# Performance work log

Hardware: AMD Instinct MI355X
Metric: run time of the kernel (lower is better)

## Reference

```python
import jax, jax.numpy as jnp
import numpy as np

B, S, H, I, E, TOPK, KS = 4, 4096, 1024, 512, 16, 2, 3


def setup_inputs() -> dict:
    key = jax.random.key(0)
    ks = jax.random.split(key, 9)
    sc = 0.02
    return {
        "hidden_states": jax.random.normal(ks[0], (B, S, H), dtype=jnp.float32),
        "router_w": jax.random.normal(ks[1], (H, E), dtype=jnp.float32) * sc,
        "router_bias": jnp.zeros((E,), dtype=jnp.float32),
        "expert_gate_w": jax.random.normal(ks[2], (E - 1, H, I), dtype=jnp.float32) * sc,
        "expert_up_w": jax.random.normal(ks[3], (E - 1, H, I), dtype=jnp.float32) * sc,
        "expert_down_w": jax.random.normal(ks[4], (E - 1, I, H), dtype=jnp.float32) * sc,
        "conv_w": jax.random.normal(ks[5], (I, H, KS), dtype=jnp.float32) * sc,
        "shared_up_w": jax.random.normal(ks[6], (H, I), dtype=jnp.float32) * sc,
        "shared_down_w": jax.random.normal(ks[7], (I, H), dtype=jnp.float32) * sc,
    }


def reference(hidden_states, router_w, router_bias, expert_gate_w, expert_up_w,
              expert_down_w, conv_w, shared_up_w, shared_down_w):
    b, s, h = hidden_states.shape
    flat = hidden_states.reshape(b * s, h)  # (T, H)

    # ---- Router (mlp type, temperature=1, no noise at eval) ----
    logits = (flat @ router_w).astype(jnp.float32) + router_bias  # (T, E)
    probs = jax.nn.softmax(logits, axis=-1)
    top_w, top_i = jax.lax.top_k(probs, TOPK)  # (T, K)
    norm_w = top_w / (jnp.sum(top_w, axis=-1, keepdims=True) + 1e-6)
    norm_w = norm_w.astype(hidden_states.dtype)
    # Dense combine weights (T, E): scatter top-k weights into expert slots
    combine = jnp.sum(jax.nn.one_hot(top_i, E, dtype=norm_w.dtype) * norm_w[..., None], axis=1)

    # ---- Routed experts: E-1 SwiGLU MLPs + 1 Identity (index E-1) ----
    routed = combine[:, E - 1:E] * flat  # identity expert contribution
    for e in range(E - 1):
        y = (jax.nn.silu(flat @ expert_gate_w[e]) * (flat @ expert_up_w[e])) @ expert_down_w[e]
        routed = routed + combine[:, e:e + 1] * y
    routed = routed.reshape(b, s, h)

    # ---- Shared expert: causal conv1d gate * up, then down ----
    x_ncw = jnp.transpose(hidden_states, (0, 2, 1))  # (B, H, S)
    gate = jax.lax.conv_general_dilated(
        x_ncw, conv_w, window_strides=(1,), padding=[(KS - 1, 0)],
        dimension_numbers=("NCW", "OIW", "NCW"))  # (B, I, S)
    gate = jnp.transpose(gate, (0, 2, 1))  # (B, S, I)
    shared = (jax.nn.silu(gate) * (hidden_states @ shared_up_w)) @ shared_down_w

    return shared + routed
```

## Files before the change

### kernel.cpp

```cpp
#include <hip/hip_runtime.h>

typedef unsigned short u16;
typedef __attribute__((ext_vector_type(4))) float f32x4;
using bf16x8 = __attribute__((ext_vector_type(8))) short;
typedef __attribute__((ext_vector_type(8))) unsigned short u16x8;
typedef __attribute__((ext_vector_type(4))) unsigned short u16x4;

#define GAS __attribute__((address_space(1)))
#define LAS __attribute__((address_space(3)))

__device__ __forceinline__ float bf2f(u16 u) {
  unsigned v = ((unsigned)u) << 16;
  float f;
  __builtin_memcpy(&f, &v, 4);
  return f;
}
__device__ __forceinline__ u16 f2bf(float f) {
  unsigned u;
  __builtin_memcpy(&u, &f, 4);
  u += 0x7fffu + ((u >> 16) & 1u);
  return (u16)(u >> 16);
}
__device__ __forceinline__ void llds16(const void* g, void* l) {
  __builtin_amdgcn_global_load_lds((const GAS unsigned*)g, (LAS unsigned*)l, 16, 0, 0);
}

__global__ __launch_bounds__(256) void router_k(const float* __restrict__ x,
    const float* __restrict__ rw, const float* __restrict__ rb,
    int* __restrict__ topk_idx, float* __restrict__ topk_w, int* __restrict__ ib,
    u16* __restrict__ xb) {
  __shared__ float xs[4][32 * 65];
  __shared__ float wsm[4][32 * 16];
  __shared__ float part[4][64 * 17];
  __shared__ int cnt[16];
  const int tid = threadIdx.x;
  const int wv = __builtin_amdgcn_readfirstlane(tid >> 6);
  const int lane = tid & 63;
  const int tok0 = blockIdx.x * 64;
  const int rr = lane >> 3;
  const int c4 = (lane & 7) * 4;

  float acc[16];
#pragma unroll
  for (int e = 0; e < 16; ++e) acc[e] = 0.f;

  for (int c = 0; c < 8; ++c) {
    const int hb = wv * 256 + c * 32;
    {
      f32x4 wa = *(const f32x4*)(rw + hb * 16 + lane * 4);
      f32x4 wb = *(const f32x4*)(rw + hb * 16 + 256 + lane * 4);
      *(f32x4*)&wsm[wv][lane * 4] = wa;
      *(f32x4*)&wsm[wv][256 + lane * 4] = wb;
    }
#pragma unroll
    for (int i = 0; i < 8; ++i) {
      const int row = i * 8 + rr;
      const long gb = (long)(tok0 + row) * 1024 + hb + c4;
      f32x4 v = *(const f32x4*)(x + gb);
      u16x4 b4;
#pragma unroll
      for (int j = 0; j < 4; ++j) {
        xs[wv][(c4 + j) * 65 + row] = v[j];
        b4[j] = f2bf(v[j]);
      }
      *(u16x4*)(xb + gb) = b4;
    }
    __syncthreads();
#pragma unroll
    for (int h = 0; h < 32; ++h) {
      const float xv = xs[wv][h * 65 + lane];
      const float* wrow = &wsm[wv][h * 16];
#pragma unroll
      for (int q = 0; q < 4; ++q) {
        f32x4 w4 = *(const f32x4*)(wrow + q * 4);
#pragma unroll
        for (int e = 0; e < 4; ++e) acc[q * 4 + e] += xv * w4[e];
      }
    }
    __syncthreads();
  }
#pragma unroll
  for (int e = 0; e < 16; ++e) part[wv][lane * 17 + e] = acc[e];
  if (tid < 16) cnt[tid] = 0;
  __syncthreads();
  if (tid < 64) {
    float p[16];
#pragma unroll
    for (int e = 0; e < 16; ++e)
      p[e] = part[0][tid * 17 + e] + part[1][tid * 17 + e] +
             part[2][tid * 17 + e] + part[3][tid * 17 + e] + rb[e];
    float mx = p[0];
#pragma unroll
    for (int e = 1; e < 16; ++e) mx = fmaxf(mx, p[e]);
    float sum = 0.f;
#pragma unroll
    for (int e = 0; e < 16; ++e) { p[e] = __expf(p[e] - mx); sum += p[e]; }
    int i0 = 0; float p0 = p[0];
    for (int e = 1; e < 16; ++e) if (p[e] > p0) { p0 = p[e]; i0 = e; }
    int i1 = -1; float p1 = -1.f;
    for (int e = 0; e < 16; ++e) if (e != i0 && p[e] > p1) { p1 = p[e]; i1 = e; }
    const float inv = 1.f / sum;
    p0 *= inv; p1 *= inv;
    const float d = p0 + p1 + 1e-6f;
    const int t = tok0 + tid;
    topk_idx[t * 2] = i0; topk_idx[t * 2 + 1] = i1;
    topk_w[t * 2] = p0 / d;
    topk_w[t * 2 + 1] = p1 / d;
    if (i0 < 15) atomicAdd(&cnt[i0], 1);
    if (i1 < 15) atomicAdd(&cnt[i1], 1);
  }
  __syncthreads();
  if (tid < 15 && cnt[tid] > 0) atomicAdd(&ib[tid], cnt[tid]);
}

__global__ void zero_k(int* __restrict__ ib) {
  if (threadIdx.x < 16) ib[threadIdx.x] = 0;
}

__global__ void scan_k(int* __restrict__ ib) {
  if (threadIdx.x != 0 || blockIdx.x != 0) return;
  int off = 0;
  for (int ee = 0; ee < 15; ++ee) { ib[16 + ee] = off; ib[32 + ee] = off; off += ib[ee]; }
  ib[16 + 15] = off;
  int nm = 0;
  for (int ee = 0; ee < 15; ++ee) {
    const int st = ib[16 + ee], en = ib[16 + ee + 1];
    for (int r = st; r < en; r += 128) {
      ib[64 + nm * 4] = ee; ib[64 + nm * 4 + 1] = r; ib[64 + nm * 4 + 2] = en; ++nm;
    }
  }
  ib[48] = nm;
}

__global__ __launch_bounds__(256) void scatter_k(const int* __restrict__ topk_idx,
                          const float* __restrict__ topk_w,
                          int* __restrict__ ib, int* __restrict__ tok_ids,
                          float* __restrict__ tok_w, int* __restrict__ slot_map) {
  __shared__ int cnt[16], base[16];
  const int tid = threadIdx.x;
  const int j = blockIdx.x * 256 + tid;
  if (tid < 16) cnt[tid] = 0;
  __syncthreads();
  const int e = topk_idx[j];
  int lo = 0;
  if (e < 15) lo = atomicAdd(&cnt[e], 1);
  __syncthreads();
  if (tid < 15 && cnt[tid] > 0) base[tid] = atomicAdd(&ib[32 + tid], cnt[tid]);
  __syncthreads();
  if (e < 15) {
    const int pos = base[e] + lo;
    tok_ids[pos] = j >> 1;
    tok_w[pos] = topk_w[j];
    slot_map[j] = pos;
  } else {
    slot_map[j] = -1;
  }
}

__global__ void transpose_k(const float* __restrict__ src, u16* __restrict__ dst, int R, int C) {
  __shared__ float tile[32][33];
  src += (long)blockIdx.z * R * C;
  dst += (long)blockIdx.z * R * C;
  const int c0 = blockIdx.x * 32, r0 = blockIdx.y * 32;
  const int tx = threadIdx.x & 31, ty = threadIdx.x >> 5;
#pragma unroll
  for (int i = ty; i < 32; i += 8) tile[i][tx] = src[(long)(r0 + i) * C + c0 + tx];
  __syncthreads();
#pragma unroll
  for (int i = ty; i < 32; i += 8) dst[(long)(c0 + i) * R + r0 + tx] = f2bf(tile[tx][i]);
}

__global__ void convt_k(const float* __restrict__ cw, u16* __restrict__ dst) {
  const int idx = blockIdx.x * 256 + threadIdx.x;
  if (idx >= 3 * 512 * 1024) return;
  const int k = idx >> 19;
  const int rem = idx & 524287;
  const int i = rem >> 10, h = rem & 1023;
  dst[idx] = f2bf(cw[i * 3072 + h * 3 + k]);
}

template<int V>
__global__ __launch_bounds__(256, 2)
void gemm_k(const u16* __restrict__ Abase, const u16* __restrict__ Bt0,
            const u16* __restrict__ Bt1, void* __restrict__ OUTv,
            const int* __restrict__ tbl, const int* __restrict__ nmt,
            const int* __restrict__ tok_ids, const float* __restrict__ tok_w,
            int K, int ldA, int ldOut) {
  __shared__ u16 lds[24576];
  u16* OUT = (u16*)OUTv;
  float* OUTF = (float*)OUTv;
  const int tid = threadIdx.x;
  const int wave = tid >> 6, lane = tid & 63;
  const int quad = lane >> 4, l16 = lane & 15;
  const int rA = tid >> 2;
  const int sub8 = (tid & 3) * 8;
  const int sub8s = ((tid & 3) ^ ((tid >> 3) & 3)) * 8;

  constexpr int NYC = (V == 3) ? 4 : 8;
  const int lin = (blockIdx.x & 7) * (gridDim.x >> 3) + (blockIdx.x >> 3);
  const int bx = lin / NYC, by = lin - bx * NYC;

  int e = 0, row0, row_end;
  if constexpr (V <= 1) {
    if (bx >= *nmt) return;
    e = tbl[bx * 4]; row0 = tbl[bx * 4 + 1]; row_end = tbl[bx * 4 + 2];
  } else {
    row0 = bx * 128; row_end = row0 + 128;
  }
  const int n0 = by * ((V == 0) ? 64 : 128);

  f32x4 acc[2][8];
  f32x4 acc2[2][8];
#pragma unroll
  for (int i = 0; i < 2; ++i)
#pragma unroll
    for (int j = 0; j < 8; ++j) {
      acc[i][j] = (f32x4){0.f, 0.f, 0.f, 0.f};
      if constexpr (V == 3) acc2[i][j] = (f32x4){0.f, 0.f, 0.f, 0.f};
    }

  const int swz8 = (((l16 >> 1) & 3) ^ quad) * 8;
  const int aoff0 = (wave * 32 + l16) * 32 + swz8;
  const int aoff1 = aoff0 + 512;
  const int kIters = K / 32;

  if constexpr (V != 3) {
    const u16 *pA0, *pA1, *pB0, *pB1;
    if constexpr (V == 0) {
      const int t0i = tok_ids[min(row0 + rA, row_end - 1)];
      const int t1i = tok_ids[min(row0 + rA + 64, row_end - 1)];
      pA0 = Abase + (long)t0i * 1024 + sub8s;
      pA1 = Abase + (long)t1i * 1024 + sub8s;
      pB0 = Bt0 + ((long)e * 512 + n0 + rA) * 1024 + sub8s;
      pB1 = Bt1 + ((long)e * 512 + n0 + rA) * 1024 + sub8s;
    } else if constexpr (V == 1) {
      pA0 = Abase + (long)min(row0 + rA, row_end - 1) * 512 + sub8s;
      pA1 = Abase + (long)min(row0 + rA + 64, row_end - 1) * 512 + sub8s;
      pB0 = Bt0 + ((long)e * 1024 + n0 + rA) * 512 + sub8s;
      pB1 = Bt0 + ((long)e * 1024 + n0 + rA + 64) * 512 + sub8s;
    } else {
      pA0 = Abase + (long)(row0 + rA) * ldA + sub8s;
      pA1 = Abase + (long)(row0 + rA + 64) * ldA + sub8s;
      pB0 = Bt0 + (long)(n0 + rA) * K + sub8s;
      pB1 = Bt0 + (long)(n0 + rA + 64) * K + sub8s;
    }
    auto STAGE = [&](int buf) {
      llds16(pA0, &lds[buf + wave * 512]); pA0 += 32;
      llds16(pA1, &lds[buf + 2048 + wave * 512]); pA1 += 32;
      llds16(pB0, &lds[buf + 4096 + wave * 512]); pB0 += 32;
      llds16(pB1, &lds[buf + 6144 + wave * 512]); pB1 += 32;
    };
    STAGE(0);
    STAGE(8192);
    int cur = 0, stg = 16384;
    for (int kb = 0; kb < kIters; ++kb) {
      if (kb + 1 < kIters) {
        asm volatile("s_waitcnt vmcnt(4)" ::: "memory");
      } else {
        asm volatile("s_waitcnt vmcnt(0)" ::: "memory");
      }
      __builtin_amdgcn_s_barrier();
      if (kb + 2 < kIters) {
        STAGE(stg);
        stg = (stg == 16384) ? 0 : stg + 8192;
      }
      bf16x8 a0 = *(const bf16x8*)&lds[cur + aoff0];
      bf16x8 a1 = *(const bf16x8*)&lds[cur + aoff1];
      __builtin_amdgcn_s_setprio(1);
#pragma unroll
      for (int nt = 0; nt < 8; ++nt) {
        bf16x8 b = *(const bf16x8*)&lds[cur + 4096 + (nt * 16 + l16) * 32 + swz8];
        acc[0][nt] = __builtin_amdgcn_mfma_f32_16x16x32_bf16(a0, b, acc[0][nt], 0, 0, 0);
        acc[1][nt] = __builtin_amdgcn_mfma_f32_16x16x32_bf16(a1, b, acc[1][nt], 0, 0, 0);
      }
      __builtin_amdgcn_s_setprio(0);
      cur = (cur == 16384) ? 0 : cur + 8192;
    }
    __builtin_amdgcn_s_barrier();
  } else {
    int cur = 0;
    u16x8 va0n, va1n;
    const int bb = row0 >> 12, s0 = row0 & 4095;
    for (int ph = 0; ph < 3; ++ph) {
      const u16 *pA0, *pA1, *pB0, *pB1;
      const int si0 = s0 + ph - 2 + rA;
      const bool zero0 = si0 < 0;
      pA0 = Abase + ((long)bb * 4096 + (si0 < 0 ? 0 : si0)) * 1024 + sub8s;
      pA1 = Abase + ((long)bb * 4096 + (si0 + 64)) * 1024 + sub8s;
      pB0 = Bt0 + (long)ph * 524288 + (long)(n0 + rA) * 1024 + sub8s;
      pB1 = Bt0 + (long)ph * 524288 + (long)(n0 + rA + 64) * 1024 + sub8s;

      va0n = *(const u16x8*)pA0; pA0 += 32;
      va1n = *(const u16x8*)pA1; pA1 += 32;
      if (zero0) va0n = (u16x8){0, 0, 0, 0, 0, 0, 0, 0};
      *(u16x8*)&lds[cur + rA * 32 + sub8] = va0n;
      *(u16x8*)&lds[cur + (rA + 64) * 32 + sub8] = va1n;
      llds16(pB0, &lds[cur + 4096 + wave * 512]); pB0 += 32;
      llds16(pB1, &lds[cur + 6144 + wave * 512]); pB1 += 32;
      __syncthreads();

      for (int kb = 0; kb < kIters; ++kb) {
        const int nxt = cur ^ 8192;
        const bool pre = (kb + 1 < kIters);
        if (pre) {
          llds16(pB0, &lds[nxt + 4096 + wave * 512]); pB0 += 32;
          llds16(pB1, &lds[nxt + 6144 + wave * 512]); pB1 += 32;
          va0n = *(const u16x8*)pA0; pA0 += 32;
          va1n = *(const u16x8*)pA1; pA1 += 32;
          if (zero0) va0n = (u16x8){0, 0, 0, 0, 0, 0, 0, 0};
        }
        bf16x8 a0 = *(const bf16x8*)&lds[cur + aoff0];
        bf16x8 a1 = *(const bf16x8*)&lds[cur + aoff1];
#pragma unroll
        for (int nt = 0; nt < 8; ++nt) {
          bf16x8 b = *(const bf16x8*)&lds[cur + 4096 + (nt * 16 + l16) * 32 + swz8];
          acc[0][nt] = __builtin_amdgcn_mfma_f32_16x16x32_bf16(a0, b, acc[0][nt], 0, 0, 0);
          acc[1][nt] = __builtin_amdgcn_mfma_f32_16x16x32_bf16(a1, b, acc[1][nt], 0, 0, 0);
        }
        if (pre) {
          *(u16x8*)&lds[nxt + rA * 32 + sub8] = va0n;
          *(u16x8*)&lds[nxt + (rA + 64) * 32 + sub8] = va1n;
        }
        __syncthreads();
        cur = nxt;
      }
    }
    {
      const u16* pA0 = Abase + ((long)bb * 4096 + s0 + rA) * 1024 + sub8s;
      const u16* pA1 = Abase + ((long)bb * 4096 + s0 + rA + 64) * 1024 + sub8s;
      const u16* pB0 = Bt1 + (long)(n0 + rA) * 1024 + sub8s;
      const u16* pB1 = Bt1 + (long)(n0 + rA + 64) * 1024 + sub8s;

      va0n = *(const u16x8*)pA0; pA0 += 32;
      va1n = *(const u16x8*)pA1; pA1 += 32;
      *(u16x8*)&lds[cur + rA * 32 + sub8] = va0n;
      *(u16x8*)&lds[cur + (rA + 64) * 32 + sub8] = va1n;
      llds16(pB0, &lds[cur + 4096 + wave * 512]); pB0 += 32;
      llds16(pB1, &lds[cur + 6144 + wave * 512]); pB1 += 32;
      __syncthreads();

      for (int kb = 0; kb < kIters; ++kb) {
        const int nxt = cur ^ 8192;
        const bool pre = (kb + 1 < kIters);
        if (pre) {
          llds16(pB0, &lds[nxt + 4096 + wave * 512]); pB0 += 32;
          llds16(pB1, &lds[nxt + 6144 + wave * 512]); pB1 += 32;
          va0n = *(const u16x8*)pA0; pA0 += 32;
          va1n = *(const u16x8*)pA1; pA1 += 32;
        }
        bf16x8 a0 = *(const bf16x8*)&lds[cur + aoff0];
        bf16x8 a1 = *(const bf16x8*)&lds[cur + aoff1];
#pragma unroll
        for (int nt = 0; nt < 8; ++nt) {
          bf16x8 b = *(const bf16x8*)&lds[cur + 4096 + (nt * 16 + l16) * 32 + swz8];
          acc2[0][nt] = __builtin_amdgcn_mfma_f32_16x16x32_bf16(a0, b, acc2[0][nt], 0, 0, 0);
          acc2[1][nt] = __builtin_amdgcn_mfma_f32_16x16x32_bf16(a1, b, acc2[1][nt], 0, 0, 0);
        }
        if (pre) {
          *(u16x8*)&lds[nxt + rA * 32 + sub8] = va0n;
          *(u16x8*)&lds[nxt + (rA + 64) * 32 + sub8] = va1n;
        }
        __syncthreads();
        cur = nxt;
      }
    }
  }

  const int rbase = wave * 32;
  if constexpr (V == 0) {
#pragma unroll
    for (int mt = 0; mt < 2; ++mt)
#pragma unroll
      for (int r = 0; r < 4; ++r) {
        const int row = rbase + mt * 16 + quad * 4 + r;
#pragma unroll
        for (int nt = 0; nt < 4; ++nt) {
          float g = acc[mt][nt][r], u = acc[mt][nt + 4][r];
          float sg = g / (1.f + __expf(-g));
          lds[row * 64 + nt * 16 + l16] = f2bf(sg * u);
        }
      }
    __syncthreads();
#pragma unroll
    for (int i = 0; i < 4; ++i) {
      const int c = i * 256 + tid;
      const int row = c >> 3, s8 = (c & 7) * 8;
      const int slot = row0 + row;
      if (slot < row_end)
        *(u16x8*)(OUT + (long)slot * ldOut + n0 + s8) = *(const u16x8*)&lds[row * 64 + s8];
    }
  } else if constexpr (V == 1) {
#pragma unroll
    for (int mt = 0; mt < 2; ++mt)
#pragma unroll
      for (int r = 0; r < 4; ++r) {
        const int row = rbase + mt * 16 + quad * 4 + r;
        const float wgt = tok_w[min(row0 + row, row_end - 1)];
#pragma unroll
        for (int nt = 0; nt < 8; ++nt)
          lds[row * 128 + nt * 16 + l16] = f2bf(acc[mt][nt][r] * wgt);
      }
    __syncthreads();
#pragma unroll
    for (int i = 0; i < 8; ++i) {
      const int c = i * 256 + tid;
      const int row = c >> 4, s8 = (c & 15) * 8;
      const int slot = row0 + row;
      if (slot < row_end)
        *(u16x8*)(OUT + (long)slot * ldOut + n0 + s8) = *(const u16x8*)&lds[row * 128 + s8];
    }
  } else if constexpr (V == 3) {
#pragma unroll
    for (int mt = 0; mt < 2; ++mt)
#pragma unroll
      for (int r = 0; r < 4; ++r) {
        const int row = rbase + mt * 16 + quad * 4 + r;
#pragma unroll
        for (int nt = 0; nt < 8; ++nt) {
          float g = acc[mt][nt][r], u = acc2[mt][nt][r];
          lds[row * 128 + nt * 16 + l16] = f2bf(g / (1.f + __expf(-g)) * u);
        }
      }
    __syncthreads();
#pragma unroll
    for (int i = 0; i < 8; ++i) {
      const int c = i * 256 + tid;
      const int row = c >> 4, s8 = (c & 15) * 8;
      *(u16x8*)(OUT + (long)(row0 + row) * ldOut + n0 + s8) = *(const u16x8*)&lds[row * 128 + s8];
    }
  } else {
    const u16* Yb = Bt1;
    const float* xf = (const float*)tok_ids;
    float* ldsF = (float*)lds;
#pragma unroll
    for (int p = 0; p < 2; ++p) {
      if (p) __syncthreads();
      if ((wave >> 1) == p) {
        const int lw = wave & 1;
#pragma unroll
        for (int mt = 0; mt < 2; ++mt)
#pragma unroll
          for (int r = 0; r < 4; ++r) {
            const int lrow = lw * 32 + mt * 16 + quad * 4 + r;
#pragma unroll
            for (int nt = 0; nt < 8; ++nt)
              ldsF[lrow * 128 + nt * 16 + l16] = acc[mt][nt][r];
          }
      }
      __syncthreads();
#pragma unroll
      for (int i = 0; i < 8; ++i) {
        const int c = i * 256 + tid;
        const int lrow = c >> 5, c4 = (c & 31) * 4;
        const int grow = row0 + p * 64 + lrow;
        f32x4 o = *(const f32x4*)&ldsF[lrow * 128 + c4];
        const int sm0 = tbl[grow * 2], sm1 = tbl[grow * 2 + 1];
#pragma unroll
        for (int k2 = 0; k2 < 2; ++k2) {
          const int sm = k2 ? sm1 : sm0;
          if (sm >= 0) {
            u16x4 y = *(const u16x4*)(Yb + (long)sm * 1024 + n0 + c4);
#pragma unroll
            for (int j = 0; j < 4; ++j) o[j] += bf2f(y[j]);
          } else {
            const float w = tok_w[grow * 2 + k2];
            f32x4 xv = *(const f32x4*)(xf + (long)grow * 1024 + n0 + c4);
#pragma unroll
            for (int j = 0; j < 4; ++j) o[j] += w * xv[j];
          }
        }
        *(f32x4*)(OUTF + (long)grow * ldOut + n0 + c4) = o;
      }
    }
  }
}

extern "C" void kernel_launch(void* const* d_in, const int* in_sizes, int n_in,
                              void* d_out, int out_size, void* d_ws, size_t ws_size,
                              hipStream_t stream) {
  (void)in_sizes; (void)n_in; (void)out_size; (void)ws_size;
  const float* x   = (const float*)d_in[0];
  const float* rw  = (const float*)d_in[1];
  const float* rb  = (const float*)d_in[2];
  const float* gw  = (const float*)d_in[3];
  const float* uw  = (const float*)d_in[4];
  const float* dw  = (const float*)d_in[5];
  const float* cw  = (const float*)d_in[6];
  const float* suw = (const float*)d_in[7];
  const float* sdw = (const float*)d_in[8];
  float* out = (float*)d_out;

  char* base = (char*)d_ws;
  size_t off = 0;
  auto alloc = [&](size_t b) { void* p = base + off; off = (off + b + 255) & ~(size_t)255; return p; };
  u16* xb     = (u16*)alloc(16777216ull * 2);
  u16* gate_t = (u16*)alloc(15ull * 512 * 1024 * 2);
  u16* up_t   = (u16*)alloc(15ull * 512 * 1024 * 2);
  u16* down_t = (u16*)alloc(15ull * 1024 * 512 * 2);
  u16* conv_t = (u16*)alloc(3ull * 512 * 1024 * 2);
  u16* sup_t  = (u16*)alloc(512ull * 1024 * 2);
  u16* sdn_t  = (u16*)alloc(512ull * 1024 * 2);
  u16* inter  = (u16*)alloc(32768ull * 512 * 2);
  u16* Y      = (u16*)alloc(32768ull * 1024 * 2);
  u16* UP     = (u16*)alloc(16384ull * 512 * 2);
  int*   topi    = (int*)alloc(32768 * 4);
  float* topw    = (float*)alloc(32768 * 4);
  int*   smap    = (int*)alloc(32768 * 4);
  int*   tok_ids = (int*)alloc(32768 * 4);
  float* tokw    = (float*)alloc(32768 * 4);
  int*   ib      = (int*)alloc(8192);

  zero_k<<<1, 64, 0, stream>>>(ib);
  transpose_k<<<dim3(16, 32, 15), 256, 0, stream>>>(gw, gate_t, 1024, 512);
  transpose_k<<<dim3(16, 32, 15), 256, 0, stream>>>(uw, up_t, 1024, 512);
  transpose_k<<<dim3(32, 16, 15), 256, 0, stream>>>(dw, down_t, 512, 1024);
  transpose_k<<<dim3(16, 32, 1), 256, 0, stream>>>(suw, sup_t, 1024, 512);
  transpose_k<<<dim3(32, 16, 1), 256, 0, stream>>>(sdw, sdn_t, 512, 1024);
  convt_k<<<6144, 256, 0, stream>>>(cw, conv_t);
  router_k<<<256, 256, 0, stream>>>(x, rw, rb, topi, topw, ib, xb);
  scan_k<<<1, 64, 0, stream>>>(ib);
  scatter_k<<<128, 256, 0, stream>>>(topi, topw, ib, tok_ids, tokw, smap);
  gemm_k<0><<<2176, 256, 0, stream>>>(xb, gate_t, up_t, inter, ib + 64, ib + 48,
                                      tok_ids, tokw, 1024, 1024, 512);
  gemm_k<1><<<2176, 256, 0, stream>>>(inter, down_t, nullptr, Y, ib + 64, ib + 48,
                                      nullptr, tokw, 512, 512, 1024);
  gemm_k<3><<<512, 256, 0, stream>>>(xb, conv_t, sup_t, UP, nullptr, nullptr,
                                     nullptr, nullptr, 1024, 1024, 512);
  gemm_k<4><<<1024, 256, 0, stream>>>(UP, sdn_t, Y, out, smap, nullptr,
                                      (const int*)x, topw, 512, 512, 1024);
}
```

Measured before the change: 545.4 us.

## Fuse conv taps and up projection into one K loop sharing a shifted A tile

```diff
diff --git a/kernel.cpp b/kernel.cpp
--- a/kernel.cpp
+++ b/kernel.cpp
@@ -186,17 +186,16 @@
             const int* __restrict__ tbl, const int* __restrict__ nmt,
             const int* __restrict__ tok_ids, const float* __restrict__ tok_w,
             int K, int ldA, int ldOut) {
-  __shared__ u16 lds[24576];
+  __shared__ u16 lds[24832];
   u16* OUT = (u16*)OUTv;
   float* OUTF = (float*)OUTv;
   const int tid = threadIdx.x;
   const int wave = tid >> 6, lane = tid & 63;
   const int quad = lane >> 4, l16 = lane & 15;
   const int rA = tid >> 2;
-  const int sub8 = (tid & 3) * 8;
   const int sub8s = ((tid & 3) ^ ((tid >> 3) & 3)) * 8;
 
-  constexpr int NYC = (V == 3) ? 4 : 8;
+  constexpr int NYC = 8;
   const int lin = (blockIdx.x & 7) * (gridDim.x >> 3) + (blockIdx.x >> 3);
   const int bx = lin / NYC, by = lin - bx * NYC;
 
@@ -207,17 +206,18 @@
   } else {
     row0 = bx * 128; row_end = row0 + 128;
   }
-  const int n0 = by * ((V == 0) ? 64 : 128);
+  const int n0 = by * ((V == 0 || V == 3) ? 64 : 128);
 
   f32x4 acc[2][8];
-  f32x4 acc2[2][8];
-#pragma unroll
-  for (int i = 0; i < 2; ++i)
-#pragma unroll
-    for (int j = 0; j < 8; ++j) {
-      acc[i][j] = (f32x4){0.f, 0.f, 0.f, 0.f};
-      if constexpr (V == 3) acc2[i][j] = (f32x4){0.f, 0.f, 0.f, 0.f};
-    }
+  f32x4 acc2[2][4];
+#pragma unroll
+  for (int i = 0; i < 2; ++i) {
+#pragma unroll
+    for (int j = 0; j < 8; ++j) acc[i][j] = (f32x4){0.f, 0.f, 0.f, 0.f};
+    if constexpr (V == 3)
+#pragma unroll
+      for (int j = 0; j < 4; ++j) acc2[i][j] = (f32x4){0.f, 0.f, 0.f, 0.f};
+  }
 
   const int swz8 = (((l16 >> 1) & 3) ^ quad) * 8;
   const int aoff0 = (wave * 32 + l16) * 32 + swz8;
@@ -278,91 +278,80 @@
     }
     __builtin_amdgcn_s_barrier();
   } else {
+    constexpr int BUF = 12416;
+    const int bb = row0 >> 12, s0 = row0 & 4095;
+    const int q8 = (tid & 3) * 8;
+    const int rowA0 = tid >> 2;
+    const int rowA1 = 64 + (tid >> 2);
+    const int rowAx = 128 + (tid >> 2);
+    const long xbase = (long)bb * 4096;
+    const int si0 = s0 - 2 + rowA0;
+    const bool z0 = si0 < 0;
+    const u16* pA0g = Abase + (xbase + (si0 < 0 ? 0 : si0)) * 1024 + q8;
+    const u16* pA1g = Abase + (xbase + (long)(s0 - 2 + rowA1)) * 1024 + q8;
+    const u16* pAxg = Abase + (xbase + (long)(s0 - 2 + rowAx)) * 1024 + q8;
+    const u16* pB0g = Bt0 + (long)(n0 + (tid >> 2)) * 1024 + q8;
+    const u16* pB3g = Bt1 + (long)(n0 + (tid >> 2)) * 1024 + q8;
+    u16x8 vA0, vA1, vAx;
+
     int cur = 0;
-    u16x8 va0n, va1n;
-    const int bb = row0 >> 12, s0 = row0 & 4095;
-    for (int ph = 0; ph < 3; ++ph) {
-      const u16 *pA0, *pA1, *pB0, *pB1;
-      const int si0 = s0 + ph - 2 + rA;
-      const bool zero0 = si0 < 0;
-      pA0 = Abase + ((long)bb * 4096 + (si0 < 0 ? 0 : si0)) * 1024 + sub8s;
-      pA1 = Abase + ((long)bb * 4096 + (si0 + 64)) * 1024 + sub8s;
-      pB0 = Bt0 + (long)ph * 524288 + (long)(n0 + rA) * 1024 + sub8s;
-      pB1 = Bt0 + (long)ph * 524288 + (long)(n0 + rA + 64) * 1024 + sub8s;
-
-      va0n = *(const u16x8*)pA0; pA0 += 32;
-      va1n = *(const u16x8*)pA1; pA1 += 32;
-      if (zero0) va0n = (u16x8){0, 0, 0, 0, 0, 0, 0, 0};
-      *(u16x8*)&lds[cur + rA * 32 + sub8] = va0n;
-      *(u16x8*)&lds[cur + (rA + 64) * 32 + sub8] = va1n;
-      llds16(pB0, &lds[cur + 4096 + wave * 512]); pB0 += 32;
-      llds16(pB1, &lds[cur + 6144 + wave * 512]); pB1 += 32;
+    vA0 = *(const u16x8*)pA0g;
+    vA1 = *(const u16x8*)pA1g;
+    if (tid < 8) vAx = *(const u16x8*)pAxg;
+    if (z0) vA0 = (u16x8){0, 0, 0, 0, 0, 0, 0, 0};
+    *(u16x8*)&lds[cur + rowA0 * 32 + q8] = vA0;
+    *(u16x8*)&lds[cur + rowA1 * 32 + q8] = vA1;
+    if (tid < 8) *(u16x8*)&lds[cur + rowAx * 32 + q8] = vAx;
+    llds16(pB0g, &lds[cur + 4224 + wave * 512]);
+    llds16(pB0g + 524288, &lds[cur + 4224 + 2048 + wave * 512]);
+    llds16(pB0g + 1048576, &lds[cur + 4224 + 4096 + wave * 512]);
+    llds16(pB3g, &lds[cur + 4224 + 6144 + wave * 512]);
+    __syncthreads();
+
+    for (int kb = 0; kb < kIters; ++kb) {
+      const int nxt = cur ^ BUF;
+      const bool pre = (kb + 1 < kIters);
+      const int ko = (kb + 1) * 32;
+      if (pre) {
+        llds16(pB0g + ko, &lds[nxt + 4224 + wave * 512]);
+        llds16(pB0g + 524288 + ko, &lds[nxt + 4224 + 2048 + wave * 512]);
+        llds16(pB0g + 1048576 + ko, &lds[nxt + 4224 + 4096 + wave * 512]);
+        llds16(pB3g + ko, &lds[nxt + 4224 + 6144 + wave * 512]);
+        vA0 = *(const u16x8*)(pA0g + ko);
+        vA1 = *(const u16x8*)(pA1g + ko);
+        if (tid < 8) vAx = *(const u16x8*)(pAxg + ko);
+        if (z0) vA0 = (u16x8){0, 0, 0, 0, 0, 0, 0, 0};
+      }
+      bf16x8 af00 = *(const bf16x8*)&lds[cur + (wave * 32 + 0 + l16) * 32 + quad * 8];
+      bf16x8 af01 = *(const bf16x8*)&lds[cur + (wave * 32 + 1 + l16) * 32 + quad * 8];
+      bf16x8 af02 = *(const bf16x8*)&lds[cur + (wave * 32 + 2 + l16) * 32 + quad * 8];
+      bf16x8 af10 = *(const bf16x8*)&lds[cur + (wave * 32 + 16 + l16) * 32 + quad * 8];
+      bf16x8 af11 = *(const bf16x8*)&lds[cur + (wave * 32 + 17 + l16) * 32 + quad * 8];
+      bf16x8 af12 = *(const bf16x8*)&lds[cur + (wave * 32 + 18 + l16) * 32 + quad * 8];
+      __builtin_amdgcn_s_setprio(1);
+#pragma unroll
+      for (int n = 0; n < 4; ++n) {
+        bf16x8 b0 = *(const bf16x8*)&lds[cur + 4224 + (n * 16 + l16) * 32 + quad * 8];
+        acc[0][n] = __builtin_amdgcn_mfma_f32_16x16x32_bf16(af00, b0, acc[0][n], 0, 0, 0);
+        acc[1][n] = __builtin_amdgcn_mfma_f32_16x16x32_bf16(af10, b0, acc[1][n], 0, 0, 0);
+        bf16x8 b1 = *(const bf16x8*)&lds[cur + 4224 + 2048 + (n * 16 + l16) * 32 + quad * 8];
+        acc[0][n] = __builtin_amdgcn_mfma_f32_16x16x32_bf16(af01, b1, acc[0][n], 0, 0, 0);
+        acc[1][n] = __builtin_amdgcn_mfma_f32_16x16x32_bf16(af11, b1, acc[1][n], 0, 0, 0);
+        bf16x8 b2 = *(const bf16x8*)&lds[cur + 4224 + 4096 + (n * 16 + l16) * 32 + quad * 8];
+        acc[0][n] = __builtin_amdgcn_mfma_f32_16x16x32_bf16(af02, b2, acc[0][n], 0, 0, 0);
+        acc[1][n] = __builtin_amdgcn_mfma_f32_16x16x32_bf16(af12, b2, acc[1][n], 0, 0, 0);
+        bf16x8 b3 = *(const bf16x8*)&lds[cur + 4224 + 6144 + (n * 16 + l16) * 32 + quad * 8];
+        acc2[0][n] = __builtin_amdgcn_mfma_f32_16x16x32_bf16(af02, b3, acc2[0][n], 0, 0, 0);
+        acc2[1][n] = __builtin_amdgcn_mfma_f32_16x16x32_bf16(af12, b3, acc2[1][n], 0, 0, 0);
+      }
+      __builtin_amdgcn_s_setprio(0);
+      if (pre) {
+        *(u16x8*)&lds[nxt + rowA0 * 32 + q8] = vA0;
+        *(u16x8*)&lds[nxt + rowA1 * 32 + q8] = vA1;
+        if (tid < 8) *(u16x8*)&lds[nxt + rowAx * 32 + q8] = vAx;
+      }
       __syncthreads();
-
-      for (int kb = 0; kb < kIters; ++kb) {
-        const int nxt = cur ^ 8192;
-        const bool pre = (kb + 1 < kIters);
-        if (pre) {
-          llds16(pB0, &lds[nxt + 4096 + wave * 512]); pB0 += 32;
-          llds16(pB1, &lds[nxt + 6144 + wave * 512]); pB1 += 32;
-          va0n = *(const u16x8*)pA0; pA0 += 32;
-          va1n = *(const u16x8*)pA1; pA1 += 32;
-          if (zero0) va0n = (u16x8){0, 0, 0, 0, 0, 0, 0, 0};
-        }
-        bf16x8 a0 = *(const bf16x8*)&lds[cur + aoff0];
-        bf16x8 a1 = *(const bf16x8*)&lds[cur + aoff1];
-#pragma unroll
-        for (int nt = 0; nt < 8; ++nt) {
-          bf16x8 b = *(const bf16x8*)&lds[cur + 4096 + (nt * 16 + l16) * 32 + swz8];
-          acc[0][nt] = __builtin_amdgcn_mfma_f32_16x16x32_bf16(a0, b, acc[0][nt], 0, 0, 0);
-          acc[1][nt] = __builtin_amdgcn_mfma_f32_16x16x32_bf16(a1, b, acc[1][nt], 0, 0, 0);
-        }
-        if (pre) {
-          *(u16x8*)&lds[nxt + rA * 32 + sub8] = va0n;
-          *(u16x8*)&lds[nxt + (rA + 64) * 32 + sub8] = va1n;
-        }
-        __syncthreads();
-        cur = nxt;
-      }
-    }
-    {
-      const u16* pA0 = Abase + ((long)bb * 4096 + s0 + rA) * 1024 + sub8s;
-      const u16* pA1 = Abase + ((long)bb * 4096 + s0 + rA + 64) * 1024 + sub8s;
-      const u16* pB0 = Bt1 + (long)(n0 + rA) * 1024 + sub8s;
-      const u16* pB1 = Bt1 + (long)(n0 + rA + 64) * 1024 + sub8s;
-
-      va0n = *(const u16x8*)pA0; pA0 += 32;
-      va1n = *(const u16x8*)pA1; pA1 += 32;
-      *(u16x8*)&lds[cur + rA * 32 + sub8] = va0n;
-      *(u16x8*)&lds[cur + (rA + 64) * 32 + sub8] = va1n;
-      llds16(pB0, &lds[cur + 4096 + wave * 512]); pB0 += 32;
-      llds16(pB1, &lds[cur + 6144 + wave * 512]); pB1 += 32;
-      __syncthreads();
-
-      for (int kb = 0; kb < kIters; ++kb) {
-        const int nxt = cur ^ 8192;
-        const bool pre = (kb + 1 < kIters);
-        if (pre) {
-          llds16(pB0, &lds[nxt + 4096 + wave * 512]); pB0 += 32;
-          llds16(pB1, &lds[nxt + 6144 + wave * 512]); pB1 += 32;
-          va0n = *(const u16x8*)pA0; pA0 += 32;
-          va1n = *(const u16x8*)pA1; pA1 += 32;
-        }
-        bf16x8 a0 = *(const bf16x8*)&lds[cur + aoff0];
-        bf16x8 a1 = *(const bf16x8*)&lds[cur + aoff1];
-#pragma unroll
-        for (int nt = 0; nt < 8; ++nt) {
-          bf16x8 b = *(const bf16x8*)&lds[cur + 4096 + (nt * 16 + l16) * 32 + swz8];
-          acc2[0][nt] = __builtin_amdgcn_mfma_f32_16x16x32_bf16(a0, b, acc2[0][nt], 0, 0, 0);
-          acc2[1][nt] = __builtin_amdgcn_mfma_f32_16x16x32_bf16(a1, b, acc2[1][nt], 0, 0, 0);
-        }
-        if (pre) {
-          *(u16x8*)&lds[nxt + rA * 32 + sub8] = va0n;
-          *(u16x8*)&lds[nxt + (rA + 64) * 32 + sub8] = va1n;
-        }
-        __syncthreads();
-        cur = nxt;
-      }
+      cur = nxt;
     }
   }
 
@@ -416,17 +405,17 @@
       for (int r = 0; r < 4; ++r) {
         const int row = rbase + mt * 16 + quad * 4 + r;
 #pragma unroll
-        for (int nt = 0; nt < 8; ++nt) {
-          float g = acc[mt][nt][r], u = acc2[mt][nt][r];
-          lds[row * 128 + nt * 16 + l16] = f2bf(g / (1.f + __expf(-g)) * u);
+        for (int n = 0; n < 4; ++n) {
+          float g = acc[mt][n][r], u = acc2[mt][n][r];
+          lds[row * 64 + n * 16 + l16] = f2bf(g / (1.f + __expf(-g)) * u);
         }
       }
     __syncthreads();
 #pragma unroll
-    for (int i = 0; i < 8; ++i) {
+    for (int i = 0; i < 4; ++i) {
       const int c = i * 256 + tid;
-      const int row = c >> 4, s8 = (c & 15) * 8;
-      *(u16x8*)(OUT + (long)(row0 + row) * ldOut + n0 + s8) = *(const u16x8*)&lds[row * 128 + s8];
+      const int row = c >> 3, s8 = (c & 7) * 8;
+      *(u16x8*)(OUT + (long)(row0 + row) * ldOut + n0 + s8) = *(const u16x8*)&lds[row * 64 + s8];
     }
   } else {
     const u16* Yb = Bt1;
@@ -524,8 +513,8 @@
                                       tok_ids, tokw, 1024, 1024, 512);
   gemm_k<1><<<2176, 256, 0, stream>>>(inter, down_t, nullptr, Y, ib + 64, ib + 48,
                                       nullptr, tokw, 512, 512, 1024);
-  gemm_k<3><<<512, 256, 0, stream>>>(xb, conv_t, sup_t, UP, nullptr, nullptr,
-                                     nullptr, nullptr, 1024, 1024, 512);
+  gemm_k<3><<<1024, 256, 0, stream>>>(xb, conv_t, sup_t, UP, nullptr, nullptr,
+                                      nullptr, nullptr, 1024, 1024, 512);
   gemm_k<4><<<1024, 256, 0, stream>>>(UP, sdn_t, Y, out, smap, nullptr,
                                       (const int*)x, topw, 512, 512, 1024);
 }
```

Measured after the change: 544.3 us. No clear change (-0.2%).
